# Kernel tuning notes

Hardware: AMD Instinct MI355X
Metric: run time of the kernel (lower is better)

## Reference

```python
import jax, jax.numpy as jnp
import numpy as np
from jax import lax

B, SEQ, ENC_IN, PRED = 16, 512, 321, 96
DM, DSTATE, DCONV, EXPAND, ELAYERS = 512, 16, 4, 2, 2
DI = EXPAND * DM            # 1024
DTRANK = -(-DM // 16)       # 32
EPS = 1e-5
NMAMBA = 2                  # mamba1/mamba2 shared across all encoder layers


def setup_inputs() -> dict:
    key = jax.random.key(0)
    ks = jax.random.split(key, 10)
    nrm = lambda k, sh, s=0.02: jax.random.normal(k, sh, dtype=jnp.float32) * s
    return {
        "x": jax.random.normal(ks[0], (B, SEQ, ENC_IN), dtype=jnp.float32),
        "revin_w": jnp.ones((ENC_IN,), jnp.float32),
        "revin_b": jnp.zeros((ENC_IN,), jnp.float32),
        "lin1_w": nrm(ks[1], (DM, SEQ)),
        "lin1_b": jnp.zeros((DM,), jnp.float32),
        "head_w": nrm(ks[2], (PRED, DM)),
        "head_b": jnp.zeros((PRED,), jnp.float32),
        "in_proj_w": nrm(ks[3], (NMAMBA, 2 * DI, DM)),
        "conv_w": nrm(ks[4], (NMAMBA, DI, DCONV), 0.1),
        "conv_b": jnp.zeros((NMAMBA, DI), jnp.float32),
        "x_proj_w": nrm(ks[5], (NMAMBA, DTRANK + 2 * DSTATE, DI)),
        "dt_proj_w": nrm(ks[6], (NMAMBA, DI, DTRANK), 0.1),
        "dt_proj_b": nrm(ks[7], (NMAMBA, DI), 0.1),
        "A_log": jnp.log(jnp.broadcast_to(jnp.arange(1, DSTATE + 1, dtype=jnp.float32), (NMAMBA, DI, DSTATE))),
        "D": jnp.ones((NMAMBA, DI), jnp.float32),
        "out_proj_w": nrm(ks[8], (NMAMBA, DM, DI)),
    }


def _mamba(x, ipw, cw, cb, xpw, dpw, dpb, A_log, Dp, opw):
    # x: (B, L, DM) -> (B, L, DM); standard Mamba selective-scan block
    xz = jnp.einsum('bld,ed->ble', x, ipw)            # (B,L,2*DI)
    xr, z = jnp.split(xz, 2, axis=-1)
    # causal depthwise conv over token axis L
    k = cw.T[:, None, :]                              # (DCONV,1,DI)
    xc = lax.conv_general_dilated(xr, k, window_strides=(1,), padding=[(DCONV - 1, 0)],
                                  dimension_numbers=('NHC', 'HIO', 'NHC'), feature_group_count=DI)
    xc = jax.nn.silu(xc + cb)
    dbl = jnp.einsum('bld,ed->ble', xc, xpw)          # (B,L,DTRANK+2N)
    dt, Bm, Cm = jnp.split(dbl, [DTRANK, DTRANK + DSTATE], axis=-1)
    delta = jax.nn.softplus(jnp.einsum('blr,dr->bld', dt, dpw) + dpb)  # (B,L,DI)
    A = -jnp.exp(A_log)                               # (DI,N)

    def step(h, xs):
        d_t, B_t, C_t, x_t = xs                       # (B,DI),(B,N),(B,N),(B,DI)
        dA = jnp.exp(d_t[..., None] * A)              # (B,DI,N)
        h = dA * h + (d_t * x_t)[..., None] * B_t[:, None, :]
        y = jnp.einsum('bdn,bn->bd', h, C_t)
        return h, y

    h0 = jnp.zeros((x.shape[0], DI, DSTATE), x.dtype)
    xs = (delta.transpose(1, 0, 2), Bm.transpose(1, 0, 2), Cm.transpose(1, 0, 2), xc.transpose(1, 0, 2))
    _, ys = lax.scan(step, h0, xs)
    y = ys.transpose(1, 0, 2) + Dp * xc
    y = y * jax.nn.silu(z)
    return jnp.einsum('bld,ed->ble', y, opw)


def reference(x, revin_w, revin_b, lin1_w, lin1_b, head_w, head_b,
              in_proj_w, conv_w, conv_b, x_proj_w, dt_proj_w, dt_proj_b,
              A_log, D, out_proj_w):
    # RevIN normalize (stats over time dim)
    mean = x.mean(1, keepdims=True)
    std = jnp.sqrt(x.var(1, keepdims=True) + EPS)
    xn = (x - mean) / std * revin_w + revin_b
    # channels become tokens; embed lookback window
    t = xn.transpose(0, 2, 1)                         # (B, ENC_IN, SEQ)
    t = t @ lin1_w.T + lin1_b                         # (B, ENC_IN, DM)
    p = lambda i: (in_proj_w[i], conv_w[i], conv_b[i], x_proj_w[i],
                   dt_proj_w[i], dt_proj_b[i], A_log[i], D[i], out_proj_w[i])
    for _ in range(ELAYERS):                          # mamba1/mamba2 weights shared across layers
        fwd = _mamba(t, *p(0))
        bwd = jnp.flip(_mamba(jnp.flip(t, 1), *p(1)), 1)   # is_flip bidirectional branch
        t = fwd + bwd + t
    out = t @ head_w.T + head_b                       # (B, ENC_IN, PRED)
    out = out.transpose(0, 2, 1)                      # (B, PRED, ENC_IN)
    # RevIN denorm
    out = (out - revin_b) / (revin_w + EPS * EPS)
    out = out * std + mean
    return out
```

## Files before the change

kernel.cpp:

```cpp
#include <hip/hip_runtime.h>
#include <hip/hip_bf16.h>
#include <cstdint>
#include <cstddef>

#define B_    16
#define SEQ_  512
#define CIN_  321
#define PRED_ 96
#define DM_   512
#define DI_   1024
#define NST_  16
#define RNK_  32
#define L_    321
#define NT_   (B_*CIN_)
#define PADM_ 5248
#define TC_   41
#define NC_   8
#define PS_   384

typedef unsigned short ushort_t;
typedef __bf16 bf16x8 __attribute__((ext_vector_type(8)));
typedef float  f32x4  __attribute__((ext_vector_type(4)));
typedef __attribute__((address_space(3))) void lds_void_t;
typedef const __attribute__((address_space(1))) void gbl_void_t;

__device__ __forceinline__ float sigmoidf_(float x){ return 1.f/(1.f+__expf(-x)); }
__device__ __forceinline__ float softplusf_(float x){
    return (x > 15.f) ? x : __logf(1.f + __expf(x));
}
__device__ __forceinline__ ushort_t f2bf(float f){
    union { float f; unsigned u; } v; v.f = f;
    unsigned r = v.u + 0x7FFF + ((v.u >> 16) & 1);
    return (ushort_t)(r >> 16);
}
__device__ __forceinline__ float bf2f(ushort_t u){
    return __uint_as_float(((unsigned)u) << 16);
}
__device__ __forceinline__ f32x4 bf4_to_f4(ushort4 u){
    f32x4 r; r[0]=bf2f(u.x); r[1]=bf2f(u.y); r[2]=bf2f(u.z); r[3]=bf2f(u.w);
    return r;
}

struct EpiBiasDual {
    float* C; ushort_t* Cb; const float* bias;
    __device__ void operator()(int z, int m, int n, float v) const {
        float o = v + bias[n];
        C[(size_t)m*DM_ + n] = o;
        Cb[(size_t)m*DM_ + n] = f2bf(o);
    }
};
struct EpiXZ {
    ushort_t* xzb;
    __device__ void operator()(int z, int m, int n, float v) const {
        int mm = m;
        if (z) { int b = m / L_; int l = m - b*L_; mm = b*L_ + (L_-1 - l); }
        xzb[(size_t)z*PADM_*2*DI_ + (size_t)mm*(2*DI_) + n] = f2bf(v);
    }
};
struct EpiDbl {
    float* C; ushort_t* dtb;
    __device__ void operator()(int z, int m, int n, float v) const {
        if (n < 32)
            dtb[(size_t)z*PADM_*32 + (size_t)m*32 + n] = f2bf(v);
        else if (n < 64)
            C[(size_t)z*NT_*64 + (size_t)m*64 + n] = v;
    }
};
struct EpiSpB {
    ushort_t* C; const float* bias;
    __device__ void operator()(int z, int m, int n, float v) const {
        C[(size_t)z*NT_*DI_ + (size_t)m*DI_ + n] = f2bf(softplusf_(v + bias[z*DI_ + n]));
    }
};
struct EpiP {
    ushort_t* P;
    __device__ void operator()(int z, int m, int n, float v) const {
        P[(size_t)z*NT_*DM_ + (size_t)m*DM_ + n] = f2bf(v);
    }
};
struct EpiHead {
    float* out; const float* bias; const float* mean; const float* stdv;
    const float* rw; const float* rb;
    __device__ void operator()(int z, int m, int n, float v) const {
        int b = m / CIN_, c = m - b*CIN_;
        float o = v + bias[n];
        o = (o - rb[c]) / (rw[c] + 1e-10f);
        o = o * stdv[m] + mean[m];
        out[((size_t)b*PRED_ + n)*CIN_ + c] = o;
    }
};

template<int BK, typename Epi>
__global__ __launch_bounds__(256) void gemm_bf16(const ushort_t* __restrict__ A, int lda, size_t zsa,
                                                 const ushort_t* __restrict__ Bw, int ldb, size_t zsb,
                                                 int M, int N, int K, Epi epi)
{
    __shared__ __align__(16) ushort_t As[128*BK];
    __shared__ __align__(16) ushort_t Bs[128*BK];
    const int z = blockIdx.z;
    A += (size_t)z*zsa; Bw += (size_t)z*zsb;
    const int tid  = threadIdx.x;
    const int m0 = blockIdx.x * 128, n0 = blockIdx.y * 128;
    const int wave = tid >> 6, lane = tid & 63;
    const int wm = (wave & 1) * 64, wn = (wave >> 1) * 64;
    const int ln16 = lane & 15, quad = lane >> 4;

    f32x4 acc[4][4] = {};

    if (BK == 64) {
        const int r8 = lane >> 3;
        const int colg = ((lane & 7) ^ r8) * 8;
        const ushort_t* Ag = A + (size_t)(m0 + wave*32 + r8)*lda + colg;
        const ushort_t* Bg = Bw + (size_t)(n0 + wave*32 + r8)*ldb + colg;
        ushort_t* AsW = As + wave*32*64;
        ushort_t* BsW = Bs + wave*32*64;
        for (int k0 = 0; k0 < K; k0 += 64) {
            #pragma unroll
            for (int j = 0; j < 4; ++j) {
                __builtin_amdgcn_global_load_lds((gbl_void_t*)(Ag + k0 + (size_t)(j*8)*lda),
                                                 (lds_void_t*)(AsW + j*8*64), 16, 0, 0);
                __builtin_amdgcn_global_load_lds((gbl_void_t*)(Bg + k0 + (size_t)(j*8)*ldb),
                                                 (lds_void_t*)(BsW + j*8*64), 16, 0, 0);
            }
            __syncthreads();
            #pragma unroll
            for (int ks = 0; ks < 2; ++ks) {
                bf16x8 af[4], bfr[4];
                #pragma unroll
                for (int i = 0; i < 4; ++i) {
                    int ra = wm + i*16 + ln16;
                    af[i]  = *(const bf16x8*)(As + ra*64 + (((ks*4 + quad) ^ (ra & 7)) * 8));
                    int rb2 = wn + i*16 + ln16;
                    bfr[i] = *(const bf16x8*)(Bs + rb2*64 + (((ks*4 + quad) ^ (rb2 & 7)) * 8));
                }
                #pragma unroll
                for (int mi = 0; mi < 4; ++mi)
                    #pragma unroll
                    for (int ni = 0; ni < 4; ++ni)
                        acc[mi][ni] = __builtin_amdgcn_mfma_f32_16x16x32_bf16(af[mi], bfr[ni], acc[mi][ni], 0, 0, 0);
            }
            __syncthreads();
        }
    } else {
        const int srow = lane >> 2, scol = (lane & 3) * 8;
        const ushort_t* Ag = A + (size_t)(m0 + wave*32 + srow)*lda + scol;
        const ushort_t* Bg = Bw + (size_t)(n0 + wave*32 + srow)*ldb + scol;
        ushort_t* AsW = As + wave*32*32;
        ushort_t* BsW = Bs + wave*32*32;
        for (int k0 = 0; k0 < K; k0 += 32) {
            __builtin_amdgcn_global_load_lds((gbl_void_t*)(Ag + k0),                  (lds_void_t*)AsW,           16, 0, 0);
            __builtin_amdgcn_global_load_lds((gbl_void_t*)(Ag + k0 + 16*(size_t)lda), (lds_void_t*)(AsW + 16*32), 16, 0, 0);
            __builtin_amdgcn_global_load_lds((gbl_void_t*)(Bg + k0),                  (lds_void_t*)BsW,           16, 0, 0);
            __builtin_amdgcn_global_load_lds((gbl_void_t*)(Bg + k0 + 16*(size_t)ldb), (lds_void_t*)(BsW + 16*32), 16, 0, 0);
            __syncthreads();
            bf16x8 af[4], bfr[4];
            #pragma unroll
            for (int i = 0; i < 4; ++i)
                af[i] = *(const bf16x8*)(As + (wm + i*16 + ln16)*32 + quad*8);
            #pragma unroll
            for (int i = 0; i < 4; ++i)
                bfr[i] = *(const bf16x8*)(Bs + (wn + i*16 + ln16)*32 + quad*8);
            #pragma unroll
            for (int mi = 0; mi < 4; ++mi)
                #pragma unroll
                for (int ni = 0; ni < 4; ++ni)
                    acc[mi][ni] = __builtin_amdgcn_mfma_f32_16x16x32_bf16(af[mi], bfr[ni], acc[mi][ni], 0, 0, 0);
            __syncthreads();
        }
    }

    #pragma unroll
    for (int mi = 0; mi < 4; ++mi) {
        #pragma unroll
        for (int r = 0; r < 4; ++r) {
            int m = m0 + wm + mi*16 + quad*4 + r;
            if (m >= M) continue;
            #pragma unroll
            for (int ni = 0; ni < 4; ++ni) {
                int n = n0 + wn + ni*16 + ln16;
                if (n < N) epi(z, m, n, acc[mi][ni][r]);
            }
        }
    }
}

struct CvtArgs {
    const float* src[7];
    ushort_t*    dst[7];
    int n4[7];
    int start[8];
};
__global__ __launch_bounds__(256) void cvt_all(CvtArgs a)
{
    int bid = blockIdx.x;
    int seg = 0;
    #pragma unroll
    for (int i = 0; i < 6; ++i) seg += (bid >= a.start[i+1]) ? 1 : 0;
    int idx = (bid - a.start[seg])*256 + threadIdx.x;
    if (idx < a.n4[seg]) {
        float4 v = ((const float4*)a.src[seg])[idx];
        ushort4 u; u.x=f2bf(v.x); u.y=f2bf(v.y); u.z=f2bf(v.z); u.w=f2bf(v.w);
        ((ushort4*)a.dst[seg])[idx] = u;
    }
}

__global__ __launch_bounds__(256) void revin_partial(const float* __restrict__ x,
                                                     float* __restrict__ psum,
                                                     float* __restrict__ psq)
{
    int b = blockIdx.x;
    int c0 = blockIdx.y * 64;
    int sz = blockIdx.z;
    int cl = threadIdx.x & 63;
    int sl = threadIdx.x >> 6;
    int c = c0 + cl;
    int s0 = sz * 64;
    float sum = 0.f, sq = 0.f;
    if (c < CIN_) {
        #pragma unroll
        for (int i = 0; i < 16; ++i) {
            int s = s0 + sl + i*4;
            float v = x[((size_t)b*SEQ_ + s)*CIN_ + c];
            sum += v; sq += v*v;
        }
    }
    __shared__ float ssum[4][64], ssq[4][64];
    ssum[sl][cl] = sum; ssq[sl][cl] = sq;
    __syncthreads();
    if (sl == 0 && c < CIN_) {
        float s = ssum[0][cl]+ssum[1][cl]+ssum[2][cl]+ssum[3][cl];
        float q = ssq[0][cl]+ssq[1][cl]+ssq[2][cl]+ssq[3][cl];
        psum[((size_t)b*8 + sz)*PS_ + c] = s;
        psq [((size_t)b*8 + sz)*PS_ + c] = q;
    }
}
__global__ __launch_bounds__(384) void revin_final(const float* __restrict__ psum,
                                                   const float* __restrict__ psq,
                                                   float* __restrict__ meanb,
                                                   float* __restrict__ stdb)
{
    int b = blockIdx.x;
    int c = threadIdx.x;
    if (c >= CIN_) return;
    float s = 0.f, q = 0.f;
    #pragma unroll
    for (int i = 0; i < 8; ++i) {
        s += psum[((size_t)b*8 + i)*PS_ + c];
        q += psq [((size_t)b*8 + i)*PS_ + c];
    }
    float mn = s * (1.f/SEQ_);
    float var = q * (1.f/SEQ_) - mn*mn;
    meanb[b*CIN_ + c] = mn;
    stdb[b*CIN_ + c]  = sqrtf(var + 1e-5f);
}

__global__ __launch_bounds__(256) void norm_transpose(const float* __restrict__ x,
                                                      const float* __restrict__ meanb,
                                                      const float* __restrict__ stdb,
                                                      const float* __restrict__ rw,
                                                      const float* __restrict__ rb,
                                                      ushort_t* __restrict__ xt)
{
    __shared__ float tile[64][65];
    int b = blockIdx.x, s0 = blockIdx.y*64, c0 = blockIdx.z*64;
    int cl = threadIdx.x & 63, sl = threadIdx.x >> 6;
    #pragma unroll
    for (int i = 0; i < 16; ++i) {
        int s = s0 + sl + i*4;
        int c = c0 + cl;
        float v = 0.f;
        if (c < CIN_) v = x[((size_t)b*SEQ_ + s)*CIN_ + c];
        tile[sl + i*4][cl] = v;
    }
    __syncthreads();
    int sl2 = threadIdx.x & 63, cl2 = threadIdx.x >> 6;
    #pragma unroll
    for (int i = 0; i < 16; ++i) {
        int c = c0 + cl2 + i*4;
        if (c >= CIN_) continue;
        int m = b*CIN_ + c;
        float v = tile[sl2][cl2 + i*4];
        v = (v - meanb[m]) / stdb[m] * rw[c] + rb[c];
        xt[(size_t)m*SEQ_ + s0 + sl2] = f2bf(v);
    }
}

__global__ __launch_bounds__(256) void conv_silu(const ushort_t* __restrict__ xzb,
                                                 const float* __restrict__ cw,
                                                 const float* __restrict__ cb,
                                                 ushort_t* __restrict__ xcb)
{
    int m = blockIdx.x;
    int im = blockIdx.y;
    int d4 = threadIdx.x * 4;
    const ushort_t* xz = xzb + (size_t)im*PADM_*2*DI_;
    int b = m / L_, l = m - b*L_;
    float wjt[4][4];
    #pragma unroll
    for (int j = 0; j < 4; ++j) {
        float4 w = ((const float4*)cw)[(size_t)im*DI_ + d4 + j];
        wjt[j][0]=w.x; wjt[j][1]=w.y; wjt[j][2]=w.z; wjt[j][3]=w.w;
    }
    float4 bb = *(const float4*)(cb + (size_t)im*DI_ + d4);
    float acc4[4] = {bb.x, bb.y, bb.z, bb.w};
    #pragma unroll
    for (int t = 0; t < 4; ++t) {
        int ls = l - 3 + t;
        if (ls >= 0) {
            ushort4 xv = *(const ushort4*)(xz + (size_t)(b*L_ + ls)*2*DI_ + d4);
            acc4[0] += bf2f(xv.x) * wjt[0][t];
            acc4[1] += bf2f(xv.y) * wjt[1][t];
            acc4[2] += bf2f(xv.z) * wjt[2][t];
            acc4[3] += bf2f(xv.w) * wjt[3][t];
        }
    }
    ushort4 o;
    o.x = f2bf(acc4[0] * sigmoidf_(acc4[0]));
    o.y = f2bf(acc4[1] * sigmoidf_(acc4[1]));
    o.z = f2bf(acc4[2] * sigmoidf_(acc4[2]));
    o.w = f2bf(acc4[3] * sigmoidf_(acc4[3]));
    *(ushort4*)(xcb + (size_t)im*PADM_*DI_ + (size_t)m*DI_ + d4) = o;
}


__global__ __launch_bounds__(64, 1) void scan_p1(const ushort_t* __restrict__ dl,
                                                 const ushort_t* __restrict__ xcb,
                                                 const float* __restrict__ dbl,
                                                 const float* __restrict__ A_log,
                                                 ushort_t* __restrict__ hloc,
                                                 float* __restrict__ Ssum)
{
    const int im = blockIdx.z >> 4, b = blockIdx.z & 15;
    const int c = blockIdx.y;
    const int d = blockIdx.x*64 + threadIdx.x;
    const ushort_t* dlz = dl + (size_t)im*NT_*DI_;
    const ushort_t* xcz = xcb + (size_t)im*PADM_*DI_;
    const float* dbz = dbl + (size_t)im*NT_*64;

    const float* ar = A_log + ((size_t)im*DI_ + d)*NST_;
    f32x4 t0 = *(const f32x4*)(ar+0), t1 = *(const f32x4*)(ar+4);
    f32x4 t2 = *(const f32x4*)(ar+8), t3 = *(const f32x4*)(ar+12);
    f32x4 av0, av1, av2, av3;
    #pragma unroll
    for (int j = 0; j < 4; ++j) {
        av0[j] = -__expf(t0[j]); av1[j] = -__expf(t1[j]);
        av2[j] = -__expf(t2[j]); av3[j] = -__expf(t3[j]);
    }
    const float a0 = av0[0];
    bool uni = true;
    #pragma unroll
    for (int j = 0; j < 4; ++j) {
        uni = uni && (fabsf(av0[j] - (j+1)*a0)  <= 1e-3f*(j+1));
        uni = uni && (fabsf(av1[j] - (j+5)*a0)  <= 1e-3f*(j+5));
        uni = uni && (fabsf(av2[j] - (j+9)*a0)  <= 1e-3f*(j+9));
        uni = uni && (fabsf(av3[j] - (j+13)*a0) <= 1e-3f*(j+13));
    }

    const int t0i = c*TC_, tend = (t0i + TC_ < L_) ? t0i + TC_ : L_;
    f32x4 h0 = {0,0,0,0}, h1 = {0,0,0,0}, h2 = {0,0,0,0}, h3 = {0,0,0,0};
    float S = 0.f;
    if (uni) {
        for (int t = t0i; t < tend; ++t) {
            int tok = b*L_ + t;
            float dv = bf2f(dlz[(size_t)tok*DI_ + d]);
            float xv = bf2f(xcz[(size_t)tok*DI_ + d]);
            f32x4 Bv0 = *(const f32x4*)(dbz + (size_t)tok*64 + 32);
            f32x4 Bv1 = *(const f32x4*)(dbz + (size_t)tok*64 + 36);
            f32x4 Bv2 = *(const f32x4*)(dbz + (size_t)tok*64 + 40);
            f32x4 Bv3 = *(const f32x4*)(dbz + (size_t)tok*64 + 44);
            S += dv;
            float du = dv * xv;
            float e1 = __expf(dv * a0);
            float e2 = e1*e1, e4 = e2*e2;
            f32x4 dA = {e1, e2, e2*e1, e4};
            h0 = dA*h0 + du*Bv0;  dA = dA*e4;
            h1 = dA*h1 + du*Bv1;  dA = dA*e4;
            h2 = dA*h2 + du*Bv2;  dA = dA*e4;
            h3 = dA*h3 + du*Bv3;
        }
    } else {
        for (int t = t0i; t < tend; ++t) {
            int tok = b*L_ + t;
            float dv = bf2f(dlz[(size_t)tok*DI_ + d]);
            float xv = bf2f(xcz[(size_t)tok*DI_ + d]);
            f32x4 Bv0 = *(const f32x4*)(dbz + (size_t)tok*64 + 32);
            f32x4 Bv1 = *(const f32x4*)(dbz + (size_t)tok*64 + 36);
            f32x4 Bv2 = *(const f32x4*)(dbz + (size_t)tok*64 + 40);
            f32x4 Bv3 = *(const f32x4*)(dbz + (size_t)tok*64 + 44);
            S += dv;
            float du = dv * xv;
            f32x4 dA0, dA1, dA2, dA3;
            #pragma unroll
            for (int j = 0; j < 4; ++j) {
                dA0[j] = __expf(dv*av0[j]); dA1[j] = __expf(dv*av1[j]);
                dA2[j] = __expf(dv*av2[j]); dA3[j] = __expf(dv*av3[j]);
            }
            h0 = dA0*h0 + du*Bv0;
            h1 = dA1*h1 + du*Bv1;
            h2 = dA2*h2 + du*Bv2;
            h3 = dA3*h3 + du*Bv3;
        }
    }
    size_t base = ((size_t)(im*16 + b)*NC_ + c);
    Ssum[base*DI_ + d] = S;
    #pragma unroll
    for (int n = 0; n < 4; ++n) {
        hloc[(base*NST_ + n +  0)*DI_ + d] = f2bf(h0[n]);
        hloc[(base*NST_ + n +  4)*DI_ + d] = f2bf(h1[n]);
        hloc[(base*NST_ + n +  8)*DI_ + d] = f2bf(h2[n]);
        hloc[(base*NST_ + n + 12)*DI_ + d] = f2bf(h3[n]);
    }
}

__global__ __launch_bounds__(64, 1) void scan_p2(const ushort_t* __restrict__ dl,
                                                 const ushort_t* __restrict__ xcb,
                                                 ushort_t* __restrict__ xzb,
                                                 const float* __restrict__ dbl,
                                                 const float* __restrict__ A_log,
                                                 const float* __restrict__ Dp,
                                                 const ushort_t* __restrict__ hloc,
                                                 const float* __restrict__ Ssum)
{
    const int im = blockIdx.z >> 4, b = blockIdx.z & 15;
    const int c = blockIdx.y;
    const int d = blockIdx.x*64 + threadIdx.x;
    const ushort_t* dlz = dl + (size_t)im*NT_*DI_;
    const ushort_t* xcz = xcb + (size_t)im*PADM_*DI_;
    const float* dbz = dbl + (size_t)im*NT_*64;
    ushort_t* xzz = xzb + (size_t)im*PADM_*2*DI_;

    const float* ar = A_log + ((size_t)im*DI_ + d)*NST_;
    f32x4 t0 = *(const f32x4*)(ar+0), t1 = *(const f32x4*)(ar+4);
    f32x4 t2 = *(const f32x4*)(ar+8), t3 = *(const f32x4*)(ar+12);
    f32x4 av0, av1, av2, av3;
    #pragma unroll
    for (int j = 0; j < 4; ++j) {
        av0[j] = -__expf(t0[j]); av1[j] = -__expf(t1[j]);
        av2[j] = -__expf(t2[j]); av3[j] = -__expf(t3[j]);
    }
    const float a0 = av0[0];
    bool uni = true;
    #pragma unroll
    for (int j = 0; j < 4; ++j) {
        uni = uni && (fabsf(av0[j] - (j+1)*a0)  <= 1e-3f*(j+1));
        uni = uni && (fabsf(av1[j] - (j+5)*a0)  <= 1e-3f*(j+5));
        uni = uni && (fabsf(av2[j] - (j+9)*a0)  <= 1e-3f*(j+9));
        uni = uni && (fabsf(av3[j] - (j+13)*a0) <= 1e-3f*(j+13));
    }
    const float Dd = Dp[im*DI_ + d];
    const int t0i = c*TC_, tend = (t0i + TC_ < L_) ? t0i + TC_ : L_;
    const size_t gbase = (size_t)(im*16 + b)*NC_;

    f32x4 h0 = {0,0,0,0}, h1 = {0,0,0,0}, h2 = {0,0,0,0}, h3 = {0,0,0,0};
    for (int cc = 0; cc < c; ++cc) {
        size_t base2 = gbase + cc;
        float S = Ssum[base2*DI_ + d];
        f32x4 hl0, hl1, hl2, hl3;
        #pragma unroll
        for (int n = 0; n < 4; ++n) {
            hl0[n] = bf2f(hloc[(base2*NST_ + n +  0)*DI_ + d]);
            hl1[n] = bf2f(hloc[(base2*NST_ + n +  4)*DI_ + d]);
            hl2[n] = bf2f(hloc[(base2*NST_ + n +  8)*DI_ + d]);
            hl3[n] = bf2f(hloc[(base2*NST_ + n + 12)*DI_ + d]);
        }
        if (uni) {
            float eS = __expf(S * a0);
            float e2 = eS*eS, e4 = e2*e2;
            f32x4 f = {eS, e2, e2*eS, e4};
            h0 = f*h0 + hl0;  f = f*e4;
            h1 = f*h1 + hl1;  f = f*e4;
            h2 = f*h2 + hl2;  f = f*e4;
            h3 = f*h3 + hl3;
        } else {
            f32x4 f0, f1, f2v, f3;
            #pragma unroll
            for (int j = 0; j < 4; ++j) {
                f0[j] = __expf(S*av0[j]); f1[j] = __expf(S*av1[j]);
                f2v[j] = __expf(S*av2[j]); f3[j] = __expf(S*av3[j]);
            }
            h0 = f0*h0 + hl0; h1 = f1*h1 + hl1;
            h2 = f2v*h2 + hl2; h3 = f3*h3 + hl3;
        }
    }

    if (uni) {
        for (int t = t0i; t < tend; ++t) {
            int tok = b*L_ + t;
            float dv = bf2f(dlz[(size_t)tok*DI_ + d]);
            float xv = bf2f(xcz[(size_t)tok*DI_ + d]);
            f32x4 Bv0 = *(const f32x4*)(dbz + (size_t)tok*64 + 32);
            f32x4 Bv1 = *(const f32x4*)(dbz + (size_t)tok*64 + 36);
            f32x4 Bv2 = *(const f32x4*)(dbz + (size_t)tok*64 + 40);
            f32x4 Bv3 = *(const f32x4*)(dbz + (size_t)tok*64 + 44);
            f32x4 Cv0 = *(const f32x4*)(dbz + (size_t)tok*64 + 48);
            f32x4 Cv1 = *(const f32x4*)(dbz + (size_t)tok*64 + 52);
            f32x4 Cv2 = *(const f32x4*)(dbz + (size_t)tok*64 + 56);
            f32x4 Cv3 = *(const f32x4*)(dbz + (size_t)tok*64 + 60);
            float zg = bf2f(xzz[(size_t)tok*2*DI_ + DI_ + d]);
            float du = dv * xv;
            float e1 = __expf(dv * a0);
            float e2 = e1*e1, e4 = e2*e2;
            f32x4 dA = {e1, e2, e2*e1, e4};
            h0 = dA*h0 + du*Bv0;  dA = dA*e4;
            h1 = dA*h1 + du*Bv1;  dA = dA*e4;
            h2 = dA*h2 + du*Bv2;  dA = dA*e4;
            h3 = dA*h3 + du*Bv3;
            f32x4 yv = h0*Cv0 + h1*Cv1 + h2*Cv2 + h3*Cv3;
            float y = yv[0] + yv[1] + yv[2] + yv[3];
            y = (y + Dd*xv) * (zg * sigmoidf_(zg));
            xzz[(size_t)tok*2*DI_ + d] = f2bf(y);
        }
    } else {
        for (int t = t0i; t < tend; ++t) {
            int tok = b*L_ + t;
            float dv = bf2f(dlz[(size_t)tok*DI_ + d]);
            float xv = bf2f(xcz[(size_t)tok*DI_ + d]);
            f32x4 Bv0 = *(const f32x4*)(dbz + (size_t)tok*64 + 32);
            f32x4 Bv1 = *(const f32x4*)(dbz + (size_t)tok*64 + 36);
            f32x4 Bv2 = *(const f32x4*)(dbz + (size_t)tok*64 + 40);
            f32x4 Bv3 = *(const f32x4*)(dbz + (size_t)tok*64 + 44);
            f32x4 Cv0 = *(const f32x4*)(dbz + (size_t)tok*64 + 48);
            f32x4 Cv1 = *(const f32x4*)(dbz + (size_t)tok*64 + 52);
            f32x4 Cv2 = *(const f32x4*)(dbz + (size_t)tok*64 + 56);
            f32x4 Cv3 = *(const f32x4*)(dbz + (size_t)tok*64 + 60);
            float zg = bf2f(xzz[(size_t)tok*2*DI_ + DI_ + d]);
            float du = dv * xv;
            f32x4 dA0, dA1, dA2, dA3;
            #pragma unroll
            for (int j = 0; j < 4; ++j) {
                dA0[j] = __expf(dv*av0[j]); dA1[j] = __expf(dv*av1[j]);
                dA2[j] = __expf(dv*av2[j]); dA3[j] = __expf(dv*av3[j]);
            }
            h0 = dA0*h0 + du*Bv0;
            h1 = dA1*h1 + du*Bv1;
            h2 = dA2*h2 + du*Bv2;
            h3 = dA3*h3 + du*Bv3;
            f32x4 yv = h0*Cv0 + h1*Cv1 + h2*Cv2 + h3*Cv3;
            float y = yv[0] + yv[1] + yv[2] + yv[3];
            y = (y + Dd*xv) * (zg * sigmoidf_(zg));
            xzz[(size_t)tok*2*DI_ + d] = f2bf(y);
        }
    }
}

__global__ __launch_bounds__(256) void fuse_res(float* __restrict__ t,
                                                ushort_t* __restrict__ tbf,
                                                const ushort_t* __restrict__ P)
{
    const int row4 = DM_/4;
    size_t i = (size_t)blockIdx.x*256 + threadIdx.x;
    int m = (int)(i / row4), c4 = (int)(i - (size_t)m*row4);
    int b = m / L_, l = m - b*L_;
    int mf = b*L_ + (L_-1 - l);
    float4 tv = ((float4*)t)[i];
    ushort4 p0 = ((const ushort4*)P)[(size_t)m*row4 + c4];
    ushort4 p1 = ((const ushort4*)(P + (size_t)NT_*DM_))[(size_t)mf*row4 + c4];
    tv.x += bf2f(p0.x) + bf2f(p1.x);
    tv.y += bf2f(p0.y) + bf2f(p1.y);
    tv.z += bf2f(p0.z) + bf2f(p1.z);
    tv.w += bf2f(p0.w) + bf2f(p1.w);
    ((float4*)t)[i] = tv;
    ushort4 u; u.x=f2bf(tv.x); u.y=f2bf(tv.y); u.z=f2bf(tv.z); u.w=f2bf(tv.w);
    ((ushort4*)tbf)[i] = u;
}

extern "C" void kernel_launch(void* const* d_in, const int* in_sizes, int n_in,
                              void* d_out, int out_size, void* d_ws, size_t ws_size,
                              hipStream_t stream)
{
    const float* x      = (const float*)d_in[0];
    const float* rw     = (const float*)d_in[1];
    const float* rb     = (const float*)d_in[2];
    const float* lin1_w = (const float*)d_in[3];
    const float* lin1_b = (const float*)d_in[4];
    const float* head_w = (const float*)d_in[5];
    const float* head_b = (const float*)d_in[6];
    const float* ipw    = (const float*)d_in[7];
    const float* cw     = (const float*)d_in[8];
    const float* cb     = (const float*)d_in[9];
    const float* xpw    = (const float*)d_in[10];
    const float* dpw    = (const float*)d_in[11];
    const float* dpb    = (const float*)d_in[12];
    const float* A_log  = (const float*)d_in[13];
    const float* Dp     = (const float*)d_in[14];
    const float* opw    = (const float*)d_in[15];
    float* out = (float*)d_out;

    float* ws = (float*)d_ws;
    size_t off = 0;
    auto alloc = [&](size_t nfloats) { float* p = ws + off; off += (nfloats + 63) & ~(size_t)63; return p; };
    float* meanb = alloc(NT_);
    float* stdb  = alloc(NT_);
    float* psum  = alloc((size_t)B_*8*PS_);
    float* psq   = alloc((size_t)B_*8*PS_);
    ushort_t* xnt_bf = (ushort_t*)alloc((size_t)PADM_*SEQ_/2);
    ushort_t* tbf    = (ushort_t*)alloc((size_t)PADM_*DM_/2);
    float* tres  = alloc((size_t)NT_*DM_);
    ushort_t* xzb = (ushort_t*)alloc((size_t)2*PADM_*2*DI_/2);
    ushort_t* xcb = (ushort_t*)alloc((size_t)2*PADM_*DI_/2);
    float* dl    = alloc((size_t)2*NT_*DI_);
    float* dblb  = alloc((size_t)2*NT_*64);
    ushort_t* dtb = (ushort_t*)alloc((size_t)2*PADM_*32/2);
    ushort_t* hloc = (ushort_t*)alloc((size_t)2*16*NC_*NST_*DI_/2);
    float* Ssum  = alloc((size_t)2*16*NC_*DI_);
    ushort_t* lin1_bf = (ushort_t*)alloc((size_t)DM_*SEQ_/2);
    ushort_t* head_bf = (ushort_t*)alloc((size_t)128*DM_/2);
    ushort_t* ipw_bf  = (ushort_t*)alloc((size_t)2*2*DI_*DM_/2);
    ushort_t* opw_bf  = (ushort_t*)alloc((size_t)2*DM_*DI_/2);
    ushort_t* xpw_bf  = (ushort_t*)alloc((size_t)2*128*DI_/2);
    ushort_t* dpw_bf  = (ushort_t*)alloc((size_t)2*DI_*RNK_/2);
    ushort_t* dlb = (ushort_t*)dl;
    ushort_t* Pb  = (ushort_t*)dl;
    (void)ws_size; (void)in_sizes; (void)n_in; (void)out_size;

    dim3 blk(256);

    CvtArgs ca;
    const float* srcs[7] = {lin1_w, head_w, ipw, opw, dpw, xpw, xpw + 64*DI_};
    ushort_t*    dsts[7] = {lin1_bf, head_bf, ipw_bf, opw_bf, dpw_bf, xpw_bf, xpw_bf + 128*DI_};
    int ns[7] = {DM_*SEQ_, PRED_*DM_, 2*2*DI_*DM_, 2*DM_*DI_, 2*DI_*RNK_, 64*DI_, 64*DI_};
    ca.start[0] = 0;
    for (int i = 0; i < 7; ++i) {
        ca.src[i] = srcs[i]; ca.dst[i] = dsts[i]; ca.n4[i] = ns[i]/4;
        ca.start[i+1] = ca.start[i] + (ca.n4[i] + 255)/256;
    }
    cvt_all<<<dim3(ca.start[7]), blk, 0, stream>>>(ca);

    revin_partial<<<dim3(B_, 6, 8), blk, 0, stream>>>(x, psum, psq);
    revin_final<<<dim3(B_), dim3(384), 0, stream>>>(psum, psq, meanb, stdb);
    norm_transpose<<<dim3(B_, 8, 6), blk, 0, stream>>>(x, meanb, stdb, rw, rb, xnt_bf);
    gemm_bf16<64><<<dim3(41, 4, 1), blk, 0, stream>>>(xnt_bf, SEQ_, 0, lin1_bf, SEQ_, 0,
                                                      NT_, DM_, SEQ_,
                                                      EpiBiasDual{tres, tbf, lin1_b});

    for (int layer = 0; layer < 2; ++layer) {
        gemm_bf16<64><<<dim3(41, 16, 2), blk, 0, stream>>>(
            tbf, DM_, 0, ipw_bf, DM_, (size_t)2*DI_*DM_,
            NT_, 2*DI_, DM_, EpiXZ{xzb});
        conv_silu<<<dim3(NT_, 2), blk, 0, stream>>>(xzb, cw, cb, xcb);
        gemm_bf16<64><<<dim3(41, 1, 2), blk, 0, stream>>>(
            xcb, DI_, (size_t)PADM_*DI_, xpw_bf, DI_, (size_t)128*DI_,
            NT_, 64, DI_, EpiDbl{dblb, dtb});
        gemm_bf16<32><<<dim3(41, 8, 2), blk, 0, stream>>>(
            dtb, 32, (size_t)PADM_*32, dpw_bf, 32, (size_t)DI_*RNK_,
            NT_, DI_, RNK_, EpiSpB{dlb, dpb});
        scan_p1<<<dim3(16, NC_, 32), dim3(64), 0, stream>>>(dlb, xcb, dblb, A_log, hloc, Ssum);
        scan_p2<<<dim3(16, NC_, 32), dim3(64), 0, stream>>>(dlb, xcb, xzb, dblb, A_log, Dp, hloc, Ssum);
        gemm_bf16<64><<<dim3(41, 4, 2), blk, 0, stream>>>(
            xzb, 2*DI_, (size_t)PADM_*2*DI_, opw_bf, DI_, (size_t)DM_*DI_,
            NT_, DM_, DI_, EpiP{Pb});
        fuse_res<<<dim3((NT_*DM_/4)/256), blk, 0, stream>>>(tres, tbf, Pb);
    }
    gemm_bf16<64><<<dim3(41, 1, 1), blk, 0, stream>>>(tbf, DM_, 0, head_bf, DM_, 0,
                                                      NT_, PRED_, DM_,
                                                      EpiHead{out, head_b, meanb, stdb, rw, rb});
}
```

Before: 593.2 us.

## Fuse dt_proj and softplus into scan kernels, merge in_proj GEMMs, skip last chunk

Drops the separate dt_proj GEMM that wrote a full (2, NT, DI) bf16 delta tensor. Each scan thread now preloads its 32-element dt_proj weight row and recomputes delta with softplus from the 32-wide dt low-rank vector per token, in both scan passes. The two in_proj GEMMs are merged into one wider GEMM whose epilogue routes columns to the forward or flipped buffer. scan_p1 also skips the final chunk, since its local state is never consumed. This trades extra per-token ALU work and duplicated recomputation in two passes for removing a large memory round trip and a kernel launch.

```diff
diff --git a/kernel.cpp b/kernel.cpp
--- a/kernel.cpp
+++ b/kernel.cpp
@@ -49,12 +49,13 @@
         Cb[(size_t)m*DM_ + n] = f2bf(o);
     }
 };
-struct EpiXZ {
+struct EpiXZ2 {
     ushort_t* xzb;
-    __device__ void operator()(int z, int m, int n, float v) const {
+    __device__ void operator()(int, int m, int n, float v) const {
+        int z = n >> 11, nn = n & 2047;
         int mm = m;
         if (z) { int b = m / L_; int l = m - b*L_; mm = b*L_ + (L_-1 - l); }
-        xzb[(size_t)z*PADM_*2*DI_ + (size_t)mm*(2*DI_) + n] = f2bf(v);
+        xzb[(size_t)z*PADM_*2*DI_ + (size_t)mm*(2*DI_) + nn] = f2bf(v);
     }
 };
 struct EpiDbl {
@@ -64,12 +65,6 @@
             dtb[(size_t)z*PADM_*32 + (size_t)m*32 + n] = f2bf(v);
         else if (n < 64)
             C[(size_t)z*NT_*64 + (size_t)m*64 + n] = v;
-    }
-};
-struct EpiSpB {
-    ushort_t* C; const float* bias;
-    __device__ void operator()(int z, int m, int n, float v) const {
-        C[(size_t)z*NT_*DI_ + (size_t)m*DI_ + n] = f2bf(softplusf_(v + bias[z*DI_ + n]));
     }
 };
 struct EpiP {
@@ -323,9 +318,37 @@
 }
 
 
-__global__ __launch_bounds__(64, 1) void scan_p1(const ushort_t* __restrict__ dl,
+#define SCAN_DELTA(tok)                                                           \
+    const ushort_t* dtr = dtz + (size_t)(tok)*32;                                 \
+    f32x4 q0 = bf4_to_f4(*(const ushort4*)(dtr+0));                               \
+    f32x4 q1 = bf4_to_f4(*(const ushort4*)(dtr+4));                               \
+    f32x4 q2 = bf4_to_f4(*(const ushort4*)(dtr+8));                               \
+    f32x4 q3 = bf4_to_f4(*(const ushort4*)(dtr+12));                              \
+    f32x4 q4 = bf4_to_f4(*(const ushort4*)(dtr+16));                              \
+    f32x4 q5 = bf4_to_f4(*(const ushort4*)(dtr+20));                              \
+    f32x4 q6 = bf4_to_f4(*(const ushort4*)(dtr+24));                              \
+    f32x4 q7 = bf4_to_f4(*(const ushort4*)(dtr+28));                              \
+    f32x4 qa = q0*w0 + q1*w1 + q2*w2 + q3*w3;                                     \
+    qa = qa + q4*w4 + q5*w5 + q6*w6 + q7*w7;                                      \
+    float dv = softplusf_(qa[0] + qa[1] + qa[2] + qa[3] + dpbd);
+
+#define SCAN_W_PRELOAD                                                            \
+    const ushort_t* wr = dpw_bf + ((size_t)im*DI_ + d)*RNK_;                      \
+    f32x4 w0 = bf4_to_f4(*(const ushort4*)(wr+0));                                \
+    f32x4 w1 = bf4_to_f4(*(const ushort4*)(wr+4));                                \
+    f32x4 w2 = bf4_to_f4(*(const ushort4*)(wr+8));                                \
+    f32x4 w3 = bf4_to_f4(*(const ushort4*)(wr+12));                               \
+    f32x4 w4 = bf4_to_f4(*(const ushort4*)(wr+16));                               \
+    f32x4 w5 = bf4_to_f4(*(const ushort4*)(wr+20));                               \
+    f32x4 w6 = bf4_to_f4(*(const ushort4*)(wr+24));                               \
+    f32x4 w7 = bf4_to_f4(*(const ushort4*)(wr+28));                               \
+    const float dpbd = dpb[im*DI_ + d];
+
+__global__ __launch_bounds__(64, 1) void scan_p1(const ushort_t* __restrict__ dtb,
                                                  const ushort_t* __restrict__ xcb,
                                                  const float* __restrict__ dbl,
+                                                 const ushort_t* __restrict__ dpw_bf,
+                                                 const float* __restrict__ dpb,
                                                  const float* __restrict__ A_log,
                                                  ushort_t* __restrict__ hloc,
                                                  float* __restrict__ Ssum)
@@ -333,7 +356,7 @@
     const int im = blockIdx.z >> 4, b = blockIdx.z & 15;
     const int c = blockIdx.y;
     const int d = blockIdx.x*64 + threadIdx.x;
-    const ushort_t* dlz = dl + (size_t)im*NT_*DI_;
+    const ushort_t* dtz = dtb + (size_t)im*PADM_*32;
     const ushort_t* xcz = xcb + (size_t)im*PADM_*DI_;
     const float* dbz = dbl + (size_t)im*NT_*64;
 
@@ -355,6 +378,7 @@
         uni = uni && (fabsf(av2[j] - (j+9)*a0)  <= 1e-3f*(j+9));
         uni = uni && (fabsf(av3[j] - (j+13)*a0) <= 1e-3f*(j+13));
     }
+    SCAN_W_PRELOAD
 
     const int t0i = c*TC_, tend = (t0i + TC_ < L_) ? t0i + TC_ : L_;
     f32x4 h0 = {0,0,0,0}, h1 = {0,0,0,0}, h2 = {0,0,0,0}, h3 = {0,0,0,0};
@@ -362,7 +386,7 @@
     if (uni) {
         for (int t = t0i; t < tend; ++t) {
             int tok = b*L_ + t;
-            float dv = bf2f(dlz[(size_t)tok*DI_ + d]);
+            SCAN_DELTA(tok)
             float xv = bf2f(xcz[(size_t)tok*DI_ + d]);
             f32x4 Bv0 = *(const f32x4*)(dbz + (size_t)tok*64 + 32);
             f32x4 Bv1 = *(const f32x4*)(dbz + (size_t)tok*64 + 36);
@@ -381,7 +405,7 @@
     } else {
         for (int t = t0i; t < tend; ++t) {
             int tok = b*L_ + t;
-            float dv = bf2f(dlz[(size_t)tok*DI_ + d]);
+            SCAN_DELTA(tok)
             float xv = bf2f(xcz[(size_t)tok*DI_ + d]);
             f32x4 Bv0 = *(const f32x4*)(dbz + (size_t)tok*64 + 32);
             f32x4 Bv1 = *(const f32x4*)(dbz + (size_t)tok*64 + 36);
@@ -412,10 +436,12 @@
     }
 }
 
-__global__ __launch_bounds__(64, 1) void scan_p2(const ushort_t* __restrict__ dl,
+__global__ __launch_bounds__(64, 1) void scan_p2(const ushort_t* __restrict__ dtb,
                                                  const ushort_t* __restrict__ xcb,
                                                  ushort_t* __restrict__ xzb,
                                                  const float* __restrict__ dbl,
+                                                 const ushort_t* __restrict__ dpw_bf,
+                                                 const float* __restrict__ dpb,
                                                  const float* __restrict__ A_log,
                                                  const float* __restrict__ Dp,
                                                  const ushort_t* __restrict__ hloc,
@@ -424,7 +450,7 @@
     const int im = blockIdx.z >> 4, b = blockIdx.z & 15;
     const int c = blockIdx.y;
     const int d = blockIdx.x*64 + threadIdx.x;
-    const ushort_t* dlz = dl + (size_t)im*NT_*DI_;
+    const ushort_t* dtz = dtb + (size_t)im*PADM_*32;
     const ushort_t* xcz = xcb + (size_t)im*PADM_*DI_;
     const float* dbz = dbl + (size_t)im*NT_*64;
     ushort_t* xzz = xzb + (size_t)im*PADM_*2*DI_;
@@ -447,6 +473,7 @@
         uni = uni && (fabsf(av2[j] - (j+9)*a0)  <= 1e-3f*(j+9));
         uni = uni && (fabsf(av3[j] - (j+13)*a0) <= 1e-3f*(j+13));
     }
+    SCAN_W_PRELOAD
     const float Dd = Dp[im*DI_ + d];
     const int t0i = c*TC_, tend = (t0i + TC_ < L_) ? t0i + TC_ : L_;
     const size_t gbase = (size_t)(im*16 + b)*NC_;
@@ -486,7 +513,7 @@
     if (uni) {
         for (int t = t0i; t < tend; ++t) {
             int tok = b*L_ + t;
-            float dv = bf2f(dlz[(size_t)tok*DI_ + d]);
+            SCAN_DELTA(tok)
             float xv = bf2f(xcz[(size_t)tok*DI_ + d]);
             f32x4 Bv0 = *(const f32x4*)(dbz + (size_t)tok*64 + 32);
             f32x4 Bv1 = *(const f32x4*)(dbz + (size_t)tok*64 + 36);
@@ -513,7 +540,7 @@
     } else {
         for (int t = t0i; t < tend; ++t) {
             int tok = b*L_ + t;
-            float dv = bf2f(dlz[(size_t)tok*DI_ + d]);
+            SCAN_DELTA(tok)
             float xv = bf2f(xcz[(size_t)tok*DI_ + d]);
             f32x4 Bv0 = *(const f32x4*)(dbz + (size_t)tok*64 + 32);
             f32x4 Bv1 = *(const f32x4*)(dbz + (size_t)tok*64 + 36);
@@ -598,7 +625,7 @@
     float* tres  = alloc((size_t)NT_*DM_);
     ushort_t* xzb = (ushort_t*)alloc((size_t)2*PADM_*2*DI_/2);
     ushort_t* xcb = (ushort_t*)alloc((size_t)2*PADM_*DI_/2);
-    float* dl    = alloc((size_t)2*NT_*DI_);
+    ushort_t* Pb  = (ushort_t*)alloc((size_t)2*NT_*DM_/2);
     float* dblb  = alloc((size_t)2*NT_*64);
     ushort_t* dtb = (ushort_t*)alloc((size_t)2*PADM_*32/2);
     ushort_t* hloc = (ushort_t*)alloc((size_t)2*16*NC_*NST_*DI_/2);
@@ -609,8 +636,6 @@
     ushort_t* opw_bf  = (ushort_t*)alloc((size_t)2*DM_*DI_/2);
     ushort_t* xpw_bf  = (ushort_t*)alloc((size_t)2*128*DI_/2);
     ushort_t* dpw_bf  = (ushort_t*)alloc((size_t)2*DI_*RNK_/2);
-    ushort_t* dlb = (ushort_t*)dl;
-    ushort_t* Pb  = (ushort_t*)dl;
     (void)ws_size; (void)in_sizes; (void)n_in; (void)out_size;
 
     dim3 blk(256);
@@ -634,18 +659,17 @@
                                                       EpiBiasDual{tres, tbf, lin1_b});
 
     for (int layer = 0; layer < 2; ++layer) {
-        gemm_bf16<64><<<dim3(41, 16, 2), blk, 0, stream>>>(
-            tbf, DM_, 0, ipw_bf, DM_, (size_t)2*DI_*DM_,
-            NT_, 2*DI_, DM_, EpiXZ{xzb});
+        gemm_bf16<64><<<dim3(41, 32, 1), blk, 0, stream>>>(
+            tbf, DM_, 0, ipw_bf, DM_, 0,
+            NT_, 2*2*DI_, DM_, EpiXZ2{xzb});
         conv_silu<<<dim3(NT_, 2), blk, 0, stream>>>(xzb, cw, cb, xcb);
         gemm_bf16<64><<<dim3(41, 1, 2), blk, 0, stream>>>(
             xcb, DI_, (size_t)PADM_*DI_, xpw_bf, DI_, (size_t)128*DI_,
             NT_, 64, DI_, EpiDbl{dblb, dtb});
-        gemm_bf16<32><<<dim3(41, 8, 2), blk, 0, stream>>>(
-            dtb, 32, (size_t)PADM_*32, dpw_bf, 32, (size_t)DI_*RNK_,
-            NT_, DI_, RNK_, EpiSpB{dlb, dpb});
-        scan_p1<<<dim3(16, NC_, 32), dim3(64), 0, stream>>>(dlb, xcb, dblb, A_log, hloc, Ssum);
-        scan_p2<<<dim3(16, NC_, 32), dim3(64), 0, stream>>>(dlb, xcb, xzb, dblb, A_log, Dp, hloc, Ssum);
+        scan_p1<<<dim3(16, NC_-1, 32), dim3(64), 0, stream>>>(dtb, xcb, dblb, dpw_bf, dpb,
+                                                              A_log, hloc, Ssum);
+        scan_p2<<<dim3(16, NC_, 32), dim3(64), 0, stream>>>(dtb, xcb, xzb, dblb, dpw_bf, dpb,
+                                                            A_log, Dp, hloc, Ssum);
         gemm_bf16<64><<<dim3(41, 4, 2), blk, 0, stream>>>(
             xzb, 2*DI_, (size_t)PADM_*2*DI_, opw_bf, DI_, (size_t)DM_*DI_,
             NT_, DM_, DI_, EpiP{Pb});
```

Result: slower. 606.5 us (+2.2%).

## Fuse residual into out_proj epilogues, merge in_proj launches, store B/C in bf16

Applied to the files above, without the earlier changes.

Drops the separate fuse_res kernel. The two out_proj GEMMs now accumulate straight into the fp32 residual, and the backward-branch epilogue also flips the rows and writes the bf16 copy. The two in_proj GEMMs become one launch over a doubled N, with the epilogue routing columns to each branch. The scan's B/C projections are stored as bf16 instead of fp32, and scan_p1 skips the last chunk because its state is never used. The changes save the bf16 P round-trip and cut scan memory traffic, at the cost of lower B/C precision and two serialized out_proj GEMMs that each do a read-modify-write on tres.

```diff
diff --git a/kernel.cpp b/kernel.cpp
--- a/kernel.cpp
+++ b/kernel.cpp
@@ -49,21 +49,22 @@
         Cb[(size_t)m*DM_ + n] = f2bf(o);
     }
 };
-struct EpiXZ {
+struct EpiXZ2 {
     ushort_t* xzb;
-    __device__ void operator()(int z, int m, int n, float v) const {
+    __device__ void operator()(int, int m, int n, float v) const {
+        int z = n >> 11, nn = n & 2047;
         int mm = m;
         if (z) { int b = m / L_; int l = m - b*L_; mm = b*L_ + (L_-1 - l); }
-        xzb[(size_t)z*PADM_*2*DI_ + (size_t)mm*(2*DI_) + n] = f2bf(v);
+        xzb[(size_t)z*PADM_*2*DI_ + (size_t)mm*(2*DI_) + nn] = f2bf(v);
     }
 };
 struct EpiDbl {
-    float* C; ushort_t* dtb;
+    ushort_t* dbcb; ushort_t* dtb;
     __device__ void operator()(int z, int m, int n, float v) const {
         if (n < 32)
             dtb[(size_t)z*PADM_*32 + (size_t)m*32 + n] = f2bf(v);
         else if (n < 64)
-            C[(size_t)z*NT_*64 + (size_t)m*64 + n] = v;
+            dbcb[(size_t)z*NT_*32 + (size_t)m*32 + (n-32)] = f2bf(v);
     }
 };
 struct EpiSpB {
@@ -72,10 +73,19 @@
         C[(size_t)z*NT_*DI_ + (size_t)m*DI_ + n] = f2bf(softplusf_(v + bias[z*DI_ + n]));
     }
 };
-struct EpiP {
-    ushort_t* P;
-    __device__ void operator()(int z, int m, int n, float v) const {
-        P[(size_t)z*NT_*DM_ + (size_t)m*DM_ + n] = f2bf(v);
+struct EpiAcc {
+    float* C;
+    __device__ void operator()(int, int m, int n, float v) const {
+        C[(size_t)m*DM_ + n] += v;
+    }
+};
+struct EpiAccFlipDual {
+    float* C; ushort_t* Cb;
+    __device__ void operator()(int, int m, int n, float v) const {
+        int b = m / L_; int l = m - b*L_; int mm = b*L_ + (L_-1 - l);
+        float o = C[(size_t)mm*DM_ + n] + v;
+        C[(size_t)mm*DM_ + n] = o;
+        Cb[(size_t)mm*DM_ + n] = f2bf(o);
     }
 };
 struct EpiHead {
@@ -325,7 +335,7 @@
 
 __global__ __launch_bounds__(64, 1) void scan_p1(const ushort_t* __restrict__ dl,
                                                  const ushort_t* __restrict__ xcb,
-                                                 const float* __restrict__ dbl,
+                                                 const ushort_t* __restrict__ dbcb,
                                                  const float* __restrict__ A_log,
                                                  ushort_t* __restrict__ hloc,
                                                  float* __restrict__ Ssum)
@@ -335,7 +345,7 @@
     const int d = blockIdx.x*64 + threadIdx.x;
     const ushort_t* dlz = dl + (size_t)im*NT_*DI_;
     const ushort_t* xcz = xcb + (size_t)im*PADM_*DI_;
-    const float* dbz = dbl + (size_t)im*NT_*64;
+    const ushort_t* dbz = dbcb + (size_t)im*NT_*32;
 
     const float* ar = A_log + ((size_t)im*DI_ + d)*NST_;
     f32x4 t0 = *(const f32x4*)(ar+0), t1 = *(const f32x4*)(ar+4);
@@ -364,10 +374,10 @@
             int tok = b*L_ + t;
             float dv = bf2f(dlz[(size_t)tok*DI_ + d]);
             float xv = bf2f(xcz[(size_t)tok*DI_ + d]);
-            f32x4 Bv0 = *(const f32x4*)(dbz + (size_t)tok*64 + 32);
-            f32x4 Bv1 = *(const f32x4*)(dbz + (size_t)tok*64 + 36);
-            f32x4 Bv2 = *(const f32x4*)(dbz + (size_t)tok*64 + 40);
-            f32x4 Bv3 = *(const f32x4*)(dbz + (size_t)tok*64 + 44);
+            f32x4 Bv0 = bf4_to_f4(*(const ushort4*)(dbz + (size_t)tok*32 + 0));
+            f32x4 Bv1 = bf4_to_f4(*(const ushort4*)(dbz + (size_t)tok*32 + 4));
+            f32x4 Bv2 = bf4_to_f4(*(const ushort4*)(dbz + (size_t)tok*32 + 8));
+            f32x4 Bv3 = bf4_to_f4(*(const ushort4*)(dbz + (size_t)tok*32 + 12));
             S += dv;
             float du = dv * xv;
             float e1 = __expf(dv * a0);
@@ -383,10 +393,10 @@
             int tok = b*L_ + t;
             float dv = bf2f(dlz[(size_t)tok*DI_ + d]);
             float xv = bf2f(xcz[(size_t)tok*DI_ + d]);
-            f32x4 Bv0 = *(const f32x4*)(dbz + (size_t)tok*64 + 32);
-            f32x4 Bv1 = *(const f32x4*)(dbz + (size_t)tok*64 + 36);
-            f32x4 Bv2 = *(const f32x4*)(dbz + (size_t)tok*64 + 40);
-            f32x4 Bv3 = *(const f32x4*)(dbz + (size_t)tok*64 + 44);
+            f32x4 Bv0 = bf4_to_f4(*(const ushort4*)(dbz + (size_t)tok*32 + 0));
+            f32x4 Bv1 = bf4_to_f4(*(const ushort4*)(dbz + (size_t)tok*32 + 4));
+            f32x4 Bv2 = bf4_to_f4(*(const ushort4*)(dbz + (size_t)tok*32 + 8));
+            f32x4 Bv3 = bf4_to_f4(*(const ushort4*)(dbz + (size_t)tok*32 + 12));
             S += dv;
             float du = dv * xv;
             f32x4 dA0, dA1, dA2, dA3;
@@ -415,7 +425,7 @@
 __global__ __launch_bounds__(64, 1) void scan_p2(const ushort_t* __restrict__ dl,
                                                  const ushort_t* __restrict__ xcb,
                                                  ushort_t* __restrict__ xzb,
-                                                 const float* __restrict__ dbl,
+                                                 const ushort_t* __restrict__ dbcb,
                                                  const float* __restrict__ A_log,
                                                  const float* __restrict__ Dp,
                                                  const ushort_t* __restrict__ hloc,
@@ -426,7 +436,7 @@
     const int d = blockIdx.x*64 + threadIdx.x;
     const ushort_t* dlz = dl + (size_t)im*NT_*DI_;
     const ushort_t* xcz = xcb + (size_t)im*PADM_*DI_;
-    const float* dbz = dbl + (size_t)im*NT_*64;
+    const ushort_t* dbz = dbcb + (size_t)im*NT_*32;
     ushort_t* xzz = xzb + (size_t)im*PADM_*2*DI_;
 
     const float* ar = A_log + ((size_t)im*DI_ + d)*NST_;
@@ -488,14 +498,14 @@
             int tok = b*L_ + t;
             float dv = bf2f(dlz[(size_t)tok*DI_ + d]);
             float xv = bf2f(xcz[(size_t)tok*DI_ + d]);
-            f32x4 Bv0 = *(const f32x4*)(dbz + (size_t)tok*64 + 32);
-            f32x4 Bv1 = *(const f32x4*)(dbz + (size_t)tok*64 + 36);
-            f32x4 Bv2 = *(const f32x4*)(dbz + (size_t)tok*64 + 40);
-            f32x4 Bv3 = *(const f32x4*)(dbz + (size_t)tok*64 + 44);
-            f32x4 Cv0 = *(const f32x4*)(dbz + (size_t)tok*64 + 48);
-            f32x4 Cv1 = *(const f32x4*)(dbz + (size_t)tok*64 + 52);
-            f32x4 Cv2 = *(const f32x4*)(dbz + (size_t)tok*64 + 56);
-            f32x4 Cv3 = *(const f32x4*)(dbz + (size_t)tok*64 + 60);
+            f32x4 Bv0 = bf4_to_f4(*(const ushort4*)(dbz + (size_t)tok*32 + 0));
+            f32x4 Bv1 = bf4_to_f4(*(const ushort4*)(dbz + (size_t)tok*32 + 4));
+            f32x4 Bv2 = bf4_to_f4(*(const ushort4*)(dbz + (size_t)tok*32 + 8));
+            f32x4 Bv3 = bf4_to_f4(*(const ushort4*)(dbz + (size_t)tok*32 + 12));
+            f32x4 Cv0 = bf4_to_f4(*(const ushort4*)(dbz + (size_t)tok*32 + 16));
+            f32x4 Cv1 = bf4_to_f4(*(const ushort4*)(dbz + (size_t)tok*32 + 20));
+            f32x4 Cv2 = bf4_to_f4(*(const ushort4*)(dbz + (size_t)tok*32 + 24));
+            f32x4 Cv3 = bf4_to_f4(*(const ushort4*)(dbz + (size_t)tok*32 + 28));
             float zg = bf2f(xzz[(size_t)tok*2*DI_ + DI_ + d]);
             float du = dv * xv;
             float e1 = __expf(dv * a0);
@@ -515,14 +525,14 @@
             int tok = b*L_ + t;
             float dv = bf2f(dlz[(size_t)tok*DI_ + d]);
             float xv = bf2f(xcz[(size_t)tok*DI_ + d]);
-            f32x4 Bv0 = *(const f32x4*)(dbz + (size_t)tok*64 + 32);
-            f32x4 Bv1 = *(const f32x4*)(dbz + (size_t)tok*64 + 36);
-            f32x4 Bv2 = *(const f32x4*)(dbz + (size_t)tok*64 + 40);
-            f32x4 Bv3 = *(const f32x4*)(dbz + (size_t)tok*64 + 44);
-            f32x4 Cv0 = *(const f32x4*)(dbz + (size_t)tok*64 + 48);
-            f32x4 Cv1 = *(const f32x4*)(dbz + (size_t)tok*64 + 52);
-            f32x4 Cv2 = *(const f32x4*)(dbz + (size_t)tok*64 + 56);
-            f32x4 Cv3 = *(const f32x4*)(dbz + (size_t)tok*64 + 60);
+            f32x4 Bv0 = bf4_to_f4(*(const ushort4*)(dbz + (size_t)tok*32 + 0));
+            f32x4 Bv1 = bf4_to_f4(*(const ushort4*)(dbz + (size_t)tok*32 + 4));
+            f32x4 Bv2 = bf4_to_f4(*(const ushort4*)(dbz + (size_t)tok*32 + 8));
+            f32x4 Bv3 = bf4_to_f4(*(const ushort4*)(dbz + (size_t)tok*32 + 12));
+            f32x4 Cv0 = bf4_to_f4(*(const ushort4*)(dbz + (size_t)tok*32 + 16));
+            f32x4 Cv1 = bf4_to_f4(*(const ushort4*)(dbz + (size_t)tok*32 + 20));
+            f32x4 Cv2 = bf4_to_f4(*(const ushort4*)(dbz + (size_t)tok*32 + 24));
+            f32x4 Cv3 = bf4_to_f4(*(const ushort4*)(dbz + (size_t)tok*32 + 28));
             float zg = bf2f(xzz[(size_t)tok*2*DI_ + DI_ + d]);
             float du = dv * xv;
             f32x4 dA0, dA1, dA2, dA3;
@@ -541,27 +551,6 @@
             xzz[(size_t)tok*2*DI_ + d] = f2bf(y);
         }
     }
-}
-
-__global__ __launch_bounds__(256) void fuse_res(float* __restrict__ t,
-                                                ushort_t* __restrict__ tbf,
-                                                const ushort_t* __restrict__ P)
-{
-    const int row4 = DM_/4;
-    size_t i = (size_t)blockIdx.x*256 + threadIdx.x;
-    int m = (int)(i / row4), c4 = (int)(i - (size_t)m*row4);
-    int b = m / L_, l = m - b*L_;
-    int mf = b*L_ + (L_-1 - l);
-    float4 tv = ((float4*)t)[i];
-    ushort4 p0 = ((const ushort4*)P)[(size_t)m*row4 + c4];
-    ushort4 p1 = ((const ushort4*)(P + (size_t)NT_*DM_))[(size_t)mf*row4 + c4];
-    tv.x += bf2f(p0.x) + bf2f(p1.x);
-    tv.y += bf2f(p0.y) + bf2f(p1.y);
-    tv.z += bf2f(p0.z) + bf2f(p1.z);
-    tv.w += bf2f(p0.w) + bf2f(p1.w);
-    ((float4*)t)[i] = tv;
-    ushort4 u; u.x=f2bf(tv.x); u.y=f2bf(tv.y); u.z=f2bf(tv.z); u.w=f2bf(tv.w);
-    ((ushort4*)tbf)[i] = u;
 }
 
 extern "C" void kernel_launch(void* const* d_in, const int* in_sizes, int n_in,
@@ -598,8 +587,8 @@
     float* tres  = alloc((size_t)NT_*DM_);
     ushort_t* xzb = (ushort_t*)alloc((size_t)2*PADM_*2*DI_/2);
     ushort_t* xcb = (ushort_t*)alloc((size_t)2*PADM_*DI_/2);
-    float* dl    = alloc((size_t)2*NT_*DI_);
-    float* dblb  = alloc((size_t)2*NT_*64);
+    ushort_t* dlb = (ushort_t*)alloc((size_t)2*NT_*DI_/2);
+    ushort_t* dbcb = (ushort_t*)alloc((size_t)2*NT_*32/2);
     ushort_t* dtb = (ushort_t*)alloc((size_t)2*PADM_*32/2);
     ushort_t* hloc = (ushort_t*)alloc((size_t)2*16*NC_*NST_*DI_/2);
     float* Ssum  = alloc((size_t)2*16*NC_*DI_);
@@ -609,8 +598,6 @@
     ushort_t* opw_bf  = (ushort_t*)alloc((size_t)2*DM_*DI_/2);
     ushort_t* xpw_bf  = (ushort_t*)alloc((size_t)2*128*DI_/2);
     ushort_t* dpw_bf  = (ushort_t*)alloc((size_t)2*DI_*RNK_/2);
-    ushort_t* dlb = (ushort_t*)dl;
-    ushort_t* Pb  = (ushort_t*)dl;
     (void)ws_size; (void)in_sizes; (void)n_in; (void)out_size;
 
     dim3 blk(256);
@@ -634,22 +621,24 @@
                                                       EpiBiasDual{tres, tbf, lin1_b});
 
     for (int layer = 0; layer < 2; ++layer) {
-        gemm_bf16<64><<<dim3(41, 16, 2), blk, 0, stream>>>(
-            tbf, DM_, 0, ipw_bf, DM_, (size_t)2*DI_*DM_,
-            NT_, 2*DI_, DM_, EpiXZ{xzb});
+        gemm_bf16<64><<<dim3(41, 32, 1), blk, 0, stream>>>(
+            tbf, DM_, 0, ipw_bf, DM_, 0,
+            NT_, 2*2*DI_, DM_, EpiXZ2{xzb});
         conv_silu<<<dim3(NT_, 2), blk, 0, stream>>>(xzb, cw, cb, xcb);
         gemm_bf16<64><<<dim3(41, 1, 2), blk, 0, stream>>>(
             xcb, DI_, (size_t)PADM_*DI_, xpw_bf, DI_, (size_t)128*DI_,
-            NT_, 64, DI_, EpiDbl{dblb, dtb});
+            NT_, 64, DI_, EpiDbl{dbcb, dtb});
         gemm_bf16<32><<<dim3(41, 8, 2), blk, 0, stream>>>(
             dtb, 32, (size_t)PADM_*32, dpw_bf, 32, (size_t)DI_*RNK_,
             NT_, DI_, RNK_, EpiSpB{dlb, dpb});
-        scan_p1<<<dim3(16, NC_, 32), dim3(64), 0, stream>>>(dlb, xcb, dblb, A_log, hloc, Ssum);
-        scan_p2<<<dim3(16, NC_, 32), dim3(64), 0, stream>>>(dlb, xcb, xzb, dblb, A_log, Dp, hloc, Ssum);
-        gemm_bf16<64><<<dim3(41, 4, 2), blk, 0, stream>>>(
-            xzb, 2*DI_, (size_t)PADM_*2*DI_, opw_bf, DI_, (size_t)DM_*DI_,
-            NT_, DM_, DI_, EpiP{Pb});
-        fuse_res<<<dim3((NT_*DM_/4)/256), blk, 0, stream>>>(tres, tbf, Pb);
+        scan_p1<<<dim3(16, NC_-1, 32), dim3(64), 0, stream>>>(dlb, xcb, dbcb, A_log, hloc, Ssum);
+        scan_p2<<<dim3(16, NC_, 32), dim3(64), 0, stream>>>(dlb, xcb, xzb, dbcb, A_log, Dp, hloc, Ssum);
+        gemm_bf16<64><<<dim3(41, 4, 1), blk, 0, stream>>>(
+            xzb, 2*DI_, 0, opw_bf, DI_, 0,
+            NT_, DM_, DI_, EpiAcc{tres});
+        gemm_bf16<64><<<dim3(41, 4, 1), blk, 0, stream>>>(
+            xzb + (size_t)PADM_*2*DI_, 2*DI_, 0, opw_bf + (size_t)DM_*DI_, DI_, 0,
+            NT_, DM_, DI_, EpiAccFlipDual{tres, tbf});
     }
     gemm_bf16<64><<<dim3(41, 1, 1), blk, 0, stream>>>(tbf, DM_, 0, head_bf, DM_, 0,
                                                       NT_, PRED_, DM_,
```

New measurement: 661.4 us. +11.5%, slower.
